# Optimization experiments

Measured on AMD Instinct MI355X. Metric: run time of the kernel, lower is better.

The kernel has to match this reference:

```python
import jax, jax.numpy as jnp
import numpy as np

EPS = 1e-6
L, H, D, DFF = 4, 6, 6, 64  # n_layers, num_heads(=dim, head_dim=1), d_hid, ffn hidden


def layernorm(x, w, b):
    mu = jnp.mean(x, axis=-1, keepdims=True)
    var = jnp.mean((x - mu) ** 2, axis=-1, keepdims=True)
    return (x - mu) / jnp.sqrt(var + EPS) * w + b


def autocorr(x, qw, qb, kw, kb, vw, vb, l1w, l1b):
    # x: [B,S,H]; head_dim==1 so per-head Linear is scalar w*x+b per head.
    k_in = jnp.concatenate([x[:, :1], x[:, :-1]], axis=1)   # roll right, first row kept
    v_in = jnp.concatenate([x[:, 1:], x[:, -1:]], axis=1)   # roll left, last row kept
    q = x * qw + qb
    k = k_in * kw + kb
    v = v_in * vw + vb
    teo = q * q - k * v                                      # [B,S,H]
    # nn.LayerNorm([1]) over size-1 axis: mean==x, var==0 -> output is bias
    normed = (teo - teo) / jnp.sqrt(EPS) * l1w + l1b
    scores = jax.nn.softmax(normed, axis=1)                  # over seq dim
    return scores * teo


def mha(x, p, li, ai):
    out = autocorr(x, p['qw'][li, ai], p['qb'][li, ai], p['kw'][li, ai],
                   p['kb'][li, ai], p['vw'][li, ai], p['vb'][li, ai],
                   p['ln1_w'][li, ai], p['ln1_b'][li, ai])
    return layernorm(out + x, p['mha_ln_w'][li, ai], p['mha_ln_b'][li, ai])


def setup_inputs() -> dict:
    key = jax.random.key(0)
    ks = jax.random.split(key, 24)
    n = jax.random.normal
    inp = {
        'x_batch': n(ks[0], (128, 4096, 6), jnp.float32),
        'enc_output': n(ks[1], (128, 4096, 6), jnp.float32),
        'dec_ln_w': jnp.ones((D,), jnp.float32),
        'dec_ln_b': jnp.zeros((D,), jnp.float32),
        'qw': n(ks[2], (L, 2, H), jnp.float32),
        'qb': n(ks[3], (L, 2, H), jnp.float32) * 0.1,
        'kw': n(ks[4], (L, 2, H), jnp.float32),
        'kb': n(ks[5], (L, 2, H), jnp.float32) * 0.1,
        'vw': n(ks[6], (L, 2, H), jnp.float32),
        'vb': n(ks[7], (L, 2, H), jnp.float32) * 0.1,
        'ln1_w': jnp.ones((L, 2), jnp.float32),
        'ln1_b': jnp.zeros((L, 2), jnp.float32),
        'mha_ln_w': jnp.ones((L, 2, D), jnp.float32),
        'mha_ln_b': jnp.zeros((L, 2, D), jnp.float32),
        'ffn_w1': n(ks[8], (L, DFF, D), jnp.float32) * (1.0 / np.sqrt(D)),
        'ffn_b1': jnp.zeros((L, DFF), jnp.float32),
        'ffn_w2': n(ks[9], (L, D, DFF), jnp.float32) * (1.0 / np.sqrt(DFF)),
        'ffn_b2': jnp.zeros((L, D), jnp.float32),
        'ffn_ln_w': jnp.ones((L, D), jnp.float32),
        'ffn_ln_b': jnp.zeros((L, D), jnp.float32),
    }
    return inp


def reference(x_batch, enc_output, dec_ln_w, dec_ln_b, qw, qb, kw, kb, vw, vb,
              ln1_w, ln1_b, mha_ln_w, mha_ln_b, ffn_w1, ffn_b1, ffn_w2, ffn_b2,
              ffn_ln_w, ffn_ln_b):
    p = dict(qw=qw, qb=qb, kw=kw, kb=kb, vw=vw, vb=vb, ln1_w=ln1_w, ln1_b=ln1_b,
             mha_ln_w=mha_ln_w, mha_ln_b=mha_ln_b)
    x = layernorm(x_batch, dec_ln_w, dec_ln_b)  # dropout p=0 -> identity
    for li in range(L):
        x = mha(x, p, li, 0)   # self-attention block
        x = mha(x, p, li, 1)   # "enc" attention block (also self, per source)
        h = jax.nn.relu(jnp.einsum('bsd,fd->bsf', x, ffn_w1[li]) + ffn_b1[li])
        y = jnp.einsum('bsf,df->bsd', h, ffn_w2[li]) + ffn_b2[li] + x
        x = layernorm(y, ffn_ln_w[li], ffn_ln_b[li])
    return x
```

## Files before the change

kernel.cpp:

```cpp
#include <hip/hip_runtime.h>

#define S_LEN  4096
#define DM     6
#define NLAYER 4
#define NFF    64
#define HALO   8
#define TPB    256
#define OUT_PER_WAVE 112
#define BLK_X 10

typedef float    vf2 __attribute__((ext_vector_type(2)));
typedef float    vf4 __attribute__((ext_vector_type(4)));
typedef _Float16 vh4 __attribute__((ext_vector_type(4)));

#define XSZ (128*16)
#define YSTRIDE 130
#define YSZ (6*YSTRIDE*4)
#define WAVE_LDS (XSZ + YSZ)

__device__ __forceinline__ vf2 splat2(float s){ vf2 r; r.x = s; r.y = s; return r; }
__device__ __forceinline__ unsigned pkh(float a, float b){
    return __builtin_bit_cast(unsigned, __builtin_amdgcn_cvt_pkrtz(a, b));
}

__device__ __forceinline__ void ln6v(vf2* v, const float* __restrict__ w,
                                     const float* __restrict__ b) {
    vf2 mu = (((v[0]+v[1])+(v[2]+v[3]))+(v[4]+v[5])) * (1.0f/6.0f);
    vf2 var = splat2(0.0f);
#pragma unroll
    for (int d = 0; d < DM; ++d) { vf2 dd = v[d]-mu; var = __builtin_elementwise_fma(dd, dd, var); }
    vf2 a = var * (1.0f/6.0f) + splat2(1e-6f);
    vf2 r; r.x = rsqrtf(a.x); r.y = rsqrtf(a.y);
#pragma unroll
    for (int d = 0; d < DM; ++d)
        v[d] = __builtin_elementwise_fma((v[d]-mu)*r, splat2(w[d]), splat2(b[d]));
}

__global__ __launch_bounds__(TPB)
void decoder_fused(const float* __restrict__ x_batch,
                   const float* __restrict__ dec_ln_w, const float* __restrict__ dec_ln_b,
                   const float* __restrict__ qw, const float* __restrict__ qb,
                   const float* __restrict__ kw, const float* __restrict__ kb,
                   const float* __restrict__ vw, const float* __restrict__ vb,
                   const float* __restrict__ mha_ln_w, const float* __restrict__ mha_ln_b,
                   const float* __restrict__ ffn_w1, const float* __restrict__ ffn_b1,
                   const float* __restrict__ ffn_w2, const float* __restrict__ ffn_b2,
                   const float* __restrict__ ffn_ln_w, const float* __restrict__ ffn_ln_b,
                   float* __restrict__ out) {
    const int lane = threadIdx.x & 63;
    const int wid  = threadIdx.x >> 6;
    const int w    = blockIdx.x * (TPB/64) + wid;
    const int b    = blockIdx.y;
    const int p    = w * OUT_PER_WAVE - HALO + 2*lane;
    const int c    = lane & 15, g = lane >> 4;

    __shared__ __align__(16) char smem[(TPB/64) * WAVE_LDS];
    char* wbase = smem + wid * WAVE_LDS;
    char* Xb = wbase;
    char* Yb = wbase + XSZ;

    vf2 x2[DM];
    if (p >= 0 && p + 1 < S_LEN) {
        const float4* s = reinterpret_cast<const float4*>(x_batch + ((size_t)b*S_LEN + p)*DM);
        float4 a0 = s[0], a1 = s[1], a2 = s[2];
        x2[0].x=a0.x; x2[1].x=a0.y; x2[2].x=a0.z; x2[3].x=a0.w; x2[4].x=a1.x; x2[5].x=a1.y;
        x2[0].y=a1.z; x2[1].y=a1.w; x2[2].y=a2.x; x2[3].y=a2.y; x2[4].y=a2.z; x2[5].y=a2.w;
    } else {
        const int pc = min(max(p, 0), S_LEN-1);
        const float2* s = reinterpret_cast<const float2*>(x_batch + ((size_t)b*S_LEN + pc)*DM);
        float2 a0 = s[0], a1 = s[1], a2 = s[2];
        x2[0] = splat2(a0.x); x2[1] = splat2(a0.y); x2[2] = splat2(a1.x);
        x2[3] = splat2(a1.y); x2[4] = splat2(a2.x); x2[5] = splat2(a2.y);
    }

    ln6v(x2, dec_ln_w, dec_ln_b);

#pragma unroll 1
    for (int li = 0; li < NLAYER; ++li) {
        vh4 w1f[4], w2f[4]; vf4 b1f[4];
#pragma unroll
        for (int mt = 0; mt < 4; ++mt) {
            const int f = mt*16 + c;
            float4 a = make_float4(0.f, 0.f, 0.f, 0.f);
            if (g == 0) {
                float2 u = *reinterpret_cast<const float2*>(ffn_w1 + li*NFF*DM + f*DM);
                float2 v = *reinterpret_cast<const float2*>(ffn_w1 + li*NFF*DM + f*DM + 2);
                a = make_float4(u.x, u.y, v.x, v.y);
            } else if (g == 1) {
                float2 u = *reinterpret_cast<const float2*>(ffn_w1 + li*NFF*DM + f*DM + 4);
                a = make_float4(u.x, u.y, 0.f, 0.f);
            }
            uint2 ua = make_uint2(pkh(a.x, a.y), pkh(a.z, a.w));
            w1f[mt] = __builtin_bit_cast(vh4, ua);

            float4 wv = make_float4(0.f, 0.f, 0.f, 0.f);
            if (c < DM)
                wv = *reinterpret_cast<const float4*>(ffn_w2 + li*DM*NFF + c*NFF + mt*16 + g*4);
            uint2 uw = make_uint2(pkh(wv.x, wv.y), pkh(wv.z, wv.w));
            w2f[mt] = __builtin_bit_cast(vh4, uw);

            float4 bb = *reinterpret_cast<const float4*>(ffn_b1 + li*NFF + mt*16 + g*4);
            vf4 bv; bv.x=bb.x; bv.y=bb.y; bv.z=bb.z; bv.w=bb.w;
            b1f[mt] = bv;
        }

#pragma unroll 1
        for (int ai = 0; ai < 2; ++ai) {
            const int base = (li*2 + ai) * DM;
            vf2 xm[DM], xp[DM];
#pragma unroll
            for (int d = 0; d < DM; ++d) {
                float up = __shfl_up (x2[d].y, 1);
                float dn = __shfl_down(x2[d].x, 1);
                xm[d].x = (p <= 0) ? x2[d].x : up;
                xm[d].y = x2[d].x;
                xp[d].x = x2[d].y;
                xp[d].y = (p + 1 >= S_LEN - 1) ? x2[d].y : dn;
            }
#pragma unroll
            for (int d = 0; d < DM; ++d) {
                vf2 q = __builtin_elementwise_fma(x2[d], splat2(qw[base+d]), splat2(qb[base+d]));
                vf2 k = __builtin_elementwise_fma(xm[d], splat2(kw[base+d]), splat2(kb[base+d]));
                vf2 v = __builtin_elementwise_fma(xp[d], splat2(vw[base+d]), splat2(vb[base+d]));
                vf2 teo = __builtin_elementwise_fma(q, q, -(k*v));
                x2[d] = __builtin_elementwise_fma(teo, splat2(1.0f/(float)S_LEN), x2[d]);
            }
            ln6v(x2, mha_ln_w + base, mha_ln_b + base);
        }

        {
            {
                char* r0 = Xb + lane*32;
                *(uint4*)r0      = make_uint4(pkh(x2[0].x,x2[1].x), pkh(x2[2].x,x2[3].x),
                                              pkh(x2[4].x,x2[5].x), 0u);
                *(uint4*)(r0+16) = make_uint4(pkh(x2[0].y,x2[1].y), pkh(x2[2].y,x2[3].y),
                                              pkh(x2[4].y,x2[5].y), 0u);
            }
            vh4 bfrag[8];
#pragma unroll
            for (int t = 0; t < 8; ++t) {
                vh4 v = *(const vh4*)(Xb + (16*t + c)*16 + (g&1)*8);
                if (g >= 2) v = (vh4)(_Float16)0;
                bfrag[t] = v;
            }

#pragma unroll
            for (int t = 0; t < 8; ++t) {
                vh4 hb[4];
#pragma unroll
                for (int ft = 0; ft < 4; ++ft) {
                    vf4 hc = __builtin_amdgcn_mfma_f32_16x16x16f16(w1f[ft], bfrag[t], b1f[ft], 0, 0, 0);
                    uint2 u = make_uint2(pkh(hc.x,hc.y), pkh(hc.z,hc.w));
                    vh4 hraw = __builtin_bit_cast(vh4, u);
                    vh4 z4 = (vh4)(_Float16)0;
                    hb[ft] = __builtin_elementwise_max(hraw, z4);
                }
                vf4 yacc; yacc.x=0.f; yacc.y=0.f; yacc.z=0.f; yacc.w=0.f;
#pragma unroll
                for (int ks = 0; ks < 4; ++ks)
                    yacc = __builtin_amdgcn_mfma_f32_16x16x16f16(w2f[ks], hb[ks], yacc, 0, 0, 0);
                int col = 16*t + c;
                float* yp = (float*)Yb;
                if (lane < 32) {
                    yp[(g*4+0)*YSTRIDE + col] = yacc.x;
                    yp[(g*4+1)*YSTRIDE + col] = yacc.y;
                }
                if (lane < 16) {
                    yp[2*YSTRIDE + col] = yacc.z;
                    yp[3*YSTRIDE + col] = yacc.w;
                }
            }
            const float* b2 = ffn_b2 + li*DM;
#pragma unroll
            for (int d = 0; d < DM; ++d) {
                float2 yv = *(const float2*)((float*)Yb + d*YSTRIDE + 2*lane);
                vf2 t2; t2.x = yv.x; t2.y = yv.y;
                x2[d] = x2[d] + splat2(b2[d]) + t2;
            }
            ln6v(x2, ffn_ln_w + li*DM, ffn_ln_b + li*DM);
        }
    }

    if (lane >= 4 && lane < 60 && p < S_LEN) {
        float4* dst = reinterpret_cast<float4*>(out + ((size_t)b*S_LEN + p)*DM);
        float4 a0, a1, a2;
        a0.x=x2[0].x; a0.y=x2[1].x; a0.z=x2[2].x; a0.w=x2[3].x;
        a1.x=x2[4].x; a1.y=x2[5].x; a1.z=x2[0].y; a1.w=x2[1].y;
        a2.x=x2[2].y; a2.y=x2[3].y; a2.z=x2[4].y; a2.w=x2[5].y;
        dst[0]=a0; dst[1]=a1; dst[2]=a2;
    }
}

extern "C" void kernel_launch(void* const* d_in, const int* in_sizes, int n_in,
                              void* d_out, int out_size, void* d_ws, size_t ws_size,
                              hipStream_t stream) {
    const float* x_batch  = (const float*)d_in[0];
    const float* dec_ln_w = (const float*)d_in[2];
    const float* dec_ln_b = (const float*)d_in[3];
    const float* qw       = (const float*)d_in[4];
    const float* qb       = (const float*)d_in[5];
    const float* kw       = (const float*)d_in[6];
    const float* kb       = (const float*)d_in[7];
    const float* vw       = (const float*)d_in[8];
    const float* vb       = (const float*)d_in[9];
    const float* mha_ln_w = (const float*)d_in[12];
    const float* mha_ln_b = (const float*)d_in[13];
    const float* ffn_w1   = (const float*)d_in[14];
    const float* ffn_b1   = (const float*)d_in[15];
    const float* ffn_w2   = (const float*)d_in[16];
    const float* ffn_b2   = (const float*)d_in[17];
    const float* ffn_ln_w = (const float*)d_in[18];
    const float* ffn_ln_b = (const float*)d_in[19];
    float* out = (float*)d_out;

    const int B = in_sizes[0] / (S_LEN * DM);
    dim3 grid(BLK_X, B);
    decoder_fused<<<grid, TPB, 0, stream>>>(
        x_batch, dec_ln_w, dec_ln_b, qw, qb, kw, kb, vw, vb,
        mha_ln_w, mha_ln_b, ffn_w1, ffn_b1, ffn_w2, ffn_b2,
        ffn_ln_w, ffn_ln_b, out);
}
```

Baseline: 142.3 us.

## Switch FFN to 16x16x32 f16 MFMA with transposed second GEMM

```diff
diff --git a/kernel.cpp b/kernel.cpp
--- a/kernel.cpp
+++ b/kernel.cpp
@@ -5,17 +5,18 @@
 #define NLAYER 4
 #define NFF    64
 #define HALO   8
-#define TPB    256
+#define TPB    128
 #define OUT_PER_WAVE 112
-#define BLK_X 10
+#define BLK_X 19
 
 typedef float    vf2 __attribute__((ext_vector_type(2)));
 typedef float    vf4 __attribute__((ext_vector_type(4)));
 typedef _Float16 vh4 __attribute__((ext_vector_type(4)));
+typedef _Float16 vh8 __attribute__((ext_vector_type(8)));
 
 #define XSZ (128*16)
-#define YSTRIDE 130
-#define YSZ (6*YSTRIDE*4)
+#define YSTRIDE 132
+#define YSZ (DM*YSTRIDE*4)
 #define WAVE_LDS (XSZ + YSZ)
 
 __device__ __forceinline__ vf2 splat2(float s){ vf2 r; r.x = s; r.y = s; return r; }
@@ -36,7 +37,7 @@
         v[d] = __builtin_elementwise_fma((v[d]-mu)*r, splat2(w[d]), splat2(b[d]));
 }
 
-__global__ __launch_bounds__(TPB)
+__global__ __launch_bounds__(TPB, 5)
 void decoder_fused(const float* __restrict__ x_batch,
                    const float* __restrict__ dec_ln_w, const float* __restrict__ dec_ln_b,
                    const float* __restrict__ qw, const float* __restrict__ qb,
@@ -77,31 +78,33 @@
 
 #pragma unroll 1
     for (int li = 0; li < NLAYER; ++li) {
-        vh4 w1f[4], w2f[4]; vf4 b1f[4];
+        vh8 w1f[4]; vf4 b1f[4]; vh8 w2f[2];
 #pragma unroll
         for (int mt = 0; mt < 4; ++mt) {
-            const int f = mt*16 + c;
-            float4 a = make_float4(0.f, 0.f, 0.f, 0.f);
+            uint4 ua = make_uint4(0u, 0u, 0u, 0u);
             if (g == 0) {
-                float2 u = *reinterpret_cast<const float2*>(ffn_w1 + li*NFF*DM + f*DM);
-                float2 v = *reinterpret_cast<const float2*>(ffn_w1 + li*NFF*DM + f*DM + 2);
-                a = make_float4(u.x, u.y, v.x, v.y);
-            } else if (g == 1) {
-                float2 u = *reinterpret_cast<const float2*>(ffn_w1 + li*NFF*DM + f*DM + 4);
-                a = make_float4(u.x, u.y, 0.f, 0.f);
-            }
-            uint2 ua = make_uint2(pkh(a.x, a.y), pkh(a.z, a.w));
-            w1f[mt] = __builtin_bit_cast(vh4, ua);
-
-            float4 wv = make_float4(0.f, 0.f, 0.f, 0.f);
-            if (c < DM)
-                wv = *reinterpret_cast<const float4*>(ffn_w2 + li*DM*NFF + c*NFF + mt*16 + g*4);
-            uint2 uw = make_uint2(pkh(wv.x, wv.y), pkh(wv.z, wv.w));
-            w2f[mt] = __builtin_bit_cast(vh4, uw);
+                const float* wr = ffn_w1 + li*NFF*DM + (mt*16 + c)*DM;
+                float2 u0 = *reinterpret_cast<const float2*>(wr);
+                float2 u1 = *reinterpret_cast<const float2*>(wr + 2);
+                float2 u2 = *reinterpret_cast<const float2*>(wr + 4);
+                ua = make_uint4(pkh(u0.x,u0.y), pkh(u1.x,u1.y), pkh(u2.x,u2.y), 0u);
+            }
+            w1f[mt] = __builtin_bit_cast(vh8, ua);
 
             float4 bb = *reinterpret_cast<const float4*>(ffn_b1 + li*NFF + mt*16 + g*4);
             vf4 bv; bv.x=bb.x; bv.y=bb.y; bv.z=bb.z; bv.w=bb.w;
             b1f[mt] = bv;
+        }
+#pragma unroll
+        for (int ks = 0; ks < 2; ++ks) {
+            uint4 uw = make_uint4(0u, 0u, 0u, 0u);
+            if (c < DM) {
+                const float* wr = ffn_w2 + li*DM*NFF + c*NFF + ks*32 + g*4;
+                float4 a0 = *reinterpret_cast<const float4*>(wr);
+                float4 a1 = *reinterpret_cast<const float4*>(wr + 16);
+                uw = make_uint4(pkh(a0.x,a0.y), pkh(a0.z,a0.w), pkh(a1.x,a1.y), pkh(a1.z,a1.w));
+            }
+            w2f[ks] = __builtin_bit_cast(vh8, uw);
         }
 
 #pragma unroll 1
@@ -136,38 +139,37 @@
                 *(uint4*)(r0+16) = make_uint4(pkh(x2[0].y,x2[1].y), pkh(x2[2].y,x2[3].y),
                                               pkh(x2[4].y,x2[5].y), 0u);
             }
-            vh4 bfrag[8];
+            vh8 bfrag[8];
 #pragma unroll
             for (int t = 0; t < 8; ++t) {
-                vh4 v = *(const vh4*)(Xb + (16*t + c)*16 + (g&1)*8);
-                if (g >= 2) v = (vh4)(_Float16)0;
+                vh8 v = (vh8)(_Float16)0;
+                if (g == 0) v = *(const vh8*)(Xb + (16*t + c)*16);
                 bfrag[t] = v;
             }
 
 #pragma unroll
             for (int t = 0; t < 8; ++t) {
-                vh4 hb[4];
-#pragma unroll
-                for (int ft = 0; ft < 4; ++ft) {
-                    vf4 hc = __builtin_amdgcn_mfma_f32_16x16x16f16(w1f[ft], bfrag[t], b1f[ft], 0, 0, 0);
+                unsigned P[4][2];
+#pragma unroll
+                for (int mt = 0; mt < 4; ++mt) {
+                    vf4 hc = __builtin_amdgcn_mfma_f32_16x16x32_f16(w1f[mt], bfrag[t], b1f[mt], 0, 0, 0);
                     uint2 u = make_uint2(pkh(hc.x,hc.y), pkh(hc.z,hc.w));
                     vh4 hraw = __builtin_bit_cast(vh4, u);
                     vh4 z4 = (vh4)(_Float16)0;
-                    hb[ft] = __builtin_elementwise_max(hraw, z4);
+                    vh4 hm = __builtin_elementwise_max(hraw, z4);
+                    uint2 um = __builtin_bit_cast(uint2, hm);
+                    P[mt][0] = um.x; P[mt][1] = um.y;
                 }
                 vf4 yacc; yacc.x=0.f; yacc.y=0.f; yacc.z=0.f; yacc.w=0.f;
 #pragma unroll
-                for (int ks = 0; ks < 4; ++ks)
-                    yacc = __builtin_amdgcn_mfma_f32_16x16x16f16(w2f[ks], hb[ks], yacc, 0, 0, 0);
-                int col = 16*t + c;
-                float* yp = (float*)Yb;
-                if (lane < 32) {
-                    yp[(g*4+0)*YSTRIDE + col] = yacc.x;
-                    yp[(g*4+1)*YSTRIDE + col] = yacc.y;
+                for (int ks = 0; ks < 2; ++ks) {
+                    uint4 hu = make_uint4(P[2*ks][0], P[2*ks][1], P[2*ks+1][0], P[2*ks+1][1]);
+                    vh8 hb = __builtin_bit_cast(vh8, hu);
+                    yacc = __builtin_amdgcn_mfma_f32_16x16x32_f16(hb, w2f[ks], yacc, 0, 0, 0);
                 }
-                if (lane < 16) {
-                    yp[2*YSTRIDE + col] = yacc.z;
-                    yp[3*YSTRIDE + col] = yacc.w;
+                if (c < DM) {
+                    float* yp = (float*)Yb + c*YSTRIDE + 16*t + g*4;
+                    *reinterpret_cast<vf4*>(yp) = yacc;
                 }
             }
             const float* b2 = ffn_b2 + li*DM;
```

Result: no change. 143.3 us (+0.7%).
